# Kernel tuning notes

Measured on AMD Instinct MI355X. Metric: run time of the kernel, lower is better.

Reference implementation:

```python
import jax, jax.numpy as jnp
import numpy as np

NUM_HEADS = 16

def setup_inputs() -> dict:
    key = jax.random.key(0)
    ks = jax.random.split(key, 8)
    B, S, X, D = 2, 2048, 1, 1024
    scale = 1.0 / np.sqrt(D)
    return {
        "query": jax.random.normal(ks[0], (B, S, X, D), jnp.float32),
        "key": jax.random.normal(ks[1], (B, S, X, D), jnp.float32),
        "value": jax.random.normal(ks[2], (B, S, X, D), jnp.float32),
        "Wq": jax.random.normal(ks[3], (D, D), jnp.float32) * scale,
        "bq": jnp.zeros((D,), jnp.float32),
        "Wk": jax.random.normal(ks[4], (D, D), jnp.float32) * scale,
        "bk": jnp.zeros((D,), jnp.float32),
        "Wv": jax.random.normal(ks[5], (D, D), jnp.float32) * scale,
        "bv": jnp.zeros((D,), jnp.float32),
        "Wo": jax.random.normal(ks[6], (D, D), jnp.float32) * scale,
        "bo": jnp.zeros((D,), jnp.float32),
    }

def _split_heads(x, B, H):
    # [B, S, X, D] -> [B, H, S*X, depth]
    D = x.shape[-1]
    return x.reshape(B, -1, H, D // H).transpose(0, 2, 1, 3)

def reference(query, key, value, Wq, bq, Wk, bk, Wv, bv, Wo, bo):
    B, S, X, D = query.shape
    H = NUM_HEADS
    q = _split_heads(query @ Wq + bq, B, H)   # [B,H,L,dh], L=S*X
    k = _split_heads(key @ Wk + bk, B, H)
    v = _split_heads(value @ Wv + bv, B, H)
    dh = k.shape[-1]
    logits = jnp.einsum("bhqd,bhkd->bhqk", q, k) / jnp.sqrt(jnp.float32(dh))
    attn = jax.nn.softmax(logits, axis=-1)
    out = jnp.einsum("bhqk,bhkd->bhqd", attn, v)   # [B,H,L,dh]
    out = out.transpose(0, 2, 1, 3).reshape(B, S, -1, D)  # [B,S,X,D]
    return out @ Wo + bo
```

## Files before the change

### kernel.cpp

```cpp
#include <hip/hip_runtime.h>
#include <cstdint>
#include <cstddef>

typedef _Float16 f16x8 __attribute__((ext_vector_type(8)));
typedef __fp16 fp16x2 __attribute__((ext_vector_type(2)));
typedef float f32x4 __attribute__((ext_vector_type(4)));
typedef float f32x16 __attribute__((ext_vector_type(16)));
typedef unsigned short u16;
typedef unsigned int u32;

static constexpr int Bn = 2;
static constexpr int L  = 2048;
static constexpr int Dm = 1024;
static constexpr int H  = 16;
static constexpr int DH = 64;
static constexpr int M  = Bn * L;
static constexpr size_t PER = (size_t)Bn * H * L * DH;
static constexpr int NQ = Bn * H * L;

#define SC 0.18033688f

__device__ __forceinline__ u16 f2h(float f) {
    _Float16 h = (_Float16)f;
    u16 r; __builtin_memcpy(&r, &h, 2); return r;
}
__device__ __forceinline__ u32 pk_f16(float a, float b) {
    return (u32)f2h(a) | ((u32)f2h(b) << 16);
}
__device__ __forceinline__ u32 pk_rtz(float a, float b) {
#if __has_builtin(__builtin_amdgcn_cvt_pkrtz)
    fp16x2 t = __builtin_amdgcn_cvt_pkrtz(a, b);
    u32 r; __builtin_memcpy(&r, &t, 4); return r;
#else
    return pk_f16(a, b);
#endif
}

__device__ __forceinline__ void gl2lds16(const void* g, void* l) {
    __builtin_amdgcn_global_load_lds(
        (const __attribute__((address_space(1))) u32*)(uintptr_t)g,
        (__attribute__((address_space(3))) u32*)(uintptr_t)l, 16, 0, 0);
}

__device__ __forceinline__ void drain_vm() {
    asm volatile("s_waitcnt vmcnt(0)" ::: "memory");
}

__global__ __launch_bounds__(256) void convert_in(
    const float* __restrict__ q, const float* __restrict__ k, const float* __restrict__ v,
    u16* __restrict__ dst)
{
    const float* src = (blockIdx.y == 0) ? q : (blockIdx.y == 1) ? k : v;
    u16* d = dst + (size_t)blockIdx.y * M * Dm;
    const size_t t = (size_t)blockIdx.x * 256 + threadIdx.x;
    const float4* s4 = reinterpret_cast<const float4*>(src) + t * 2;
    float4 f0 = s4[0], f1 = s4[1];
    u32 o[4] = { pk_f16(f0.x, f0.y), pk_f16(f0.z, f0.w),
                 pk_f16(f1.x, f1.y), pk_f16(f1.z, f1.w) };
    reinterpret_cast<uint4*>(d)[t] = *reinterpret_cast<uint4*>(o);
}

__global__ __launch_bounds__(256) void convert_wt(
    const float* __restrict__ Wq, const float* __restrict__ Wk,
    const float* __restrict__ Wv, const float* __restrict__ Wo,
    u16* __restrict__ dst)
{
    __shared__ u16 Ts[64][72];
    const int z = blockIdx.z;
    const float* W = (z == 0) ? Wq : (z == 1) ? Wk : (z == 2) ? Wv : Wo;
    u16* o = dst + (size_t)z * Dm * Dm;
    const int n0 = blockIdx.x * 64, k0 = blockIdx.y * 64;
    const int tid = threadIdx.x;

    {
        const int kr = tid >> 2, nc = (tid & 3) * 16;
        const float* s = W + (size_t)(k0 + kr) * Dm + n0 + nc;
        const float4* s4 = reinterpret_cast<const float4*>(s);
        float4 a = s4[0], b = s4[1], c = s4[2], d = s4[3];
        u32 t[8] = { pk_f16(a.x, a.y), pk_f16(a.z, a.w), pk_f16(b.x, b.y), pk_f16(b.z, b.w),
                     pk_f16(c.x, c.y), pk_f16(c.z, c.w), pk_f16(d.x, d.y), pk_f16(d.z, d.w) };
        *reinterpret_cast<uint4*>(&Ts[kr][nc])     = reinterpret_cast<uint4*>(t)[0];
        *reinterpret_cast<uint4*>(&Ts[kr][nc + 8]) = reinterpret_cast<uint4*>(t)[1];
    }
    __syncthreads();
    {
        const int nr = tid >> 2, kc = (tid & 3) * 16;
        u16 w[16];
        #pragma unroll
        for (int j = 0; j < 16; ++j) w[j] = Ts[kc + j][nr];
        u16* dptr = o + (size_t)(n0 + nr) * Dm + k0 + kc;
        *reinterpret_cast<uint4*>(dptr)     = reinterpret_cast<uint4*>(w)[0];
        *reinterpret_cast<uint4*>(dptr + 8) = reinterpret_cast<uint4*>(w)[1];
    }
}

__global__ __launch_bounds__(256) void gemm_qkv(
    const u16* __restrict__ Abuf, const u16* __restrict__ Wtb,
    const float* __restrict__ bq, const float* __restrict__ bk, const float* __restrict__ bv,
    u16* __restrict__ Qh, u16* __restrict__ Kh, u16* __restrict__ Vth)
{
    __shared__ __align__(16) char smem[36864];

    const int tid = threadIdx.x;
    const int wave = tid >> 6, lane = tid & 63;
    const int quad = lane >> 4, l16 = lane & 15;
    const int wr = wave >> 1, wc = wave & 1;
    const int z = blockIdx.z;
    const u16* A  = Abuf + (size_t)z * M * Dm;
    const u16* Bt = Wtb  + (size_t)z * Dm * Dm;
    const float* bias = (z == 0) ? bq : (z == 1) ? bk : bv;
    u16* out = (z == 0) ? Qh : (z == 1) ? Kh : Vth;

    const int bid = blockIdx.y * 8 + blockIdx.x;
    const int m_idx = 4 * (bid & 7) + ((bid >> 3) & 3);
    const int n_idx = bid >> 5;
    const int n0 = n_idx * 128, m0 = m_idx * 128;

    const int srow = lane >> 2;
    const int skc  = (lane & 3) * 8;

    f32x4 acc[4][4] = {};

    auto stage = [&](int k0, int bi) {
        #pragma unroll
        for (int i = 0; i < 2; ++i) {
            const int ra = i * 64 + wave * 16;
            gl2lds16(A  + (size_t)(m0 + ra + srow) * Dm + k0 + skc, smem + bi * 8192 + ra * 64);
            gl2lds16(Bt + (size_t)(n0 + ra + srow) * Dm + k0 + skc, smem + 16384 + bi * 8192 + ra * 64);
        }
    };

    stage(0, 0);
    for (int k0 = 0, it = 0; k0 < Dm; k0 += 32, ++it) {
        const int cb = it & 1;
        __syncthreads();
        if (k0 + 32 < Dm) stage(k0 + 32, cb ^ 1);
        const u16* Asb = (const u16*)(smem + cb * 8192);
        const u16* Bsb = (const u16*)(smem + 16384 + cb * 8192);
        f16x8 af[4], bf[4];
        #pragma unroll
        for (int t = 0; t < 4; ++t) {
            af[t] = *reinterpret_cast<const f16x8*>(&Asb[(wr * 64 + t * 16 + l16) * 32 + quad * 8]);
            bf[t] = *reinterpret_cast<const f16x8*>(&Bsb[(wc * 64 + t * 16 + l16) * 32 + quad * 8]);
        }
        #pragma unroll
        for (int mt = 0; mt < 4; ++mt)
            #pragma unroll
            for (int nt = 0; nt < 4; ++nt)
                acc[mt][nt] = __builtin_amdgcn_mfma_f32_16x16x32_f16(af[mt], bf[nt], acc[mt][nt], 0, 0, 0);
    }

    __syncthreads();
    u16* tile = (u16*)smem + wave * 4608;
    const float qscale = (z == 0) ? SC : 1.0f;
    #pragma unroll
    for (int nt = 0; nt < 4; ++nt) {
        const int n = n0 + wc * 64 + nt * 16 + l16;
        const float badd = bias[n];
        const int cc = nt * 16 + l16;
        #pragma unroll
        for (int mt = 0; mt < 4; ++mt) {
            #pragma unroll
            for (int r = 0; r < 4; ++r) {
                const int rr = mt * 16 + quad * 4 + r;
                const u16 vv = f2h((acc[mt][nt][r] + badd) * qscale);
                if (z == 2) tile[cc * 72 + rr] = vv;
                else        tile[rr * 72 + cc] = vv;
            }
        }
    }
    __syncthreads();

    const int rsub = lane >> 3;
    const int csub = (lane & 7) * 8;
    const int h2 = (n0 + wc * 64) >> 6;
    const int mb = m0 + wr * 64;
    const int bb = mb >> 11, ll0 = mb & 2047;
    if (z == 2) {
        const size_t baseV = ((size_t)(bb * H + h2)) * DH * L;
        #pragma unroll
        for (int j = 0; j < 8; ++j) {
            const int d = j * 8 + rsub;
            uint4 vv = *reinterpret_cast<const uint4*>(&tile[d * 72 + csub]);
            *reinterpret_cast<uint4*>(out + baseV + (size_t)d * L + ll0 + csub) = vv;
        }
    } else {
        const size_t base = ((size_t)(bb * H + h2)) * L * DH;
        #pragma unroll
        for (int j = 0; j < 8; ++j) {
            const int row = j * 8 + rsub;
            uint4 vv = *reinterpret_cast<const uint4*>(&tile[row * 72 + csub]);
            *reinterpret_cast<uint4*>(out + base + (size_t)(ll0 + row) * DH + csub) = vv;
        }
    }
}

__global__ __launch_bounds__(256) void attn(
    const u16* __restrict__ Qh, const u16* __restrict__ Kh,
    const u16* __restrict__ Vth, u16* __restrict__ Opart, float* __restrict__ rsums)
{
    __shared__ __align__(16) char smem[32768];
    u16* Os = (u16*)smem;

    const int tid  = threadIdx.x;
    const int wave = tid >> 6, lane = tid & 63;
    const int l31  = lane & 31, hh = lane >> 5;

    const int bx  = blockIdx.x;
    const int hb  = (bx & 7) | ((bx >> 8) << 3);
    const int qth = (bx >> 3) & 31;
    const int h = hb & (H - 1), b = hb >> 4;
    const int qt = qth >> 1, half = qth & 1;

    const size_t hbase = ((size_t)(b * H + h)) * L * DH;
    const int q0 = qt * 128 + wave * 32;

    u16*  Op = Opart + (size_t)half * PER;
    float* rp = rsums + (size_t)half * NQ;

    f16x8 qf[4];
    {
        const u16* qp = Qh + hbase + (size_t)(q0 + l31) * DH + hh * 8;
        #pragma unroll
        for (int c = 0; c < 4; ++c)
            qf[c] = *reinterpret_cast<const f16x8*>(qp + c * 16);
    }

    f16x8 ones;
    {
        u32 ov[4] = { 0x3C003C00u, 0x3C003C00u, 0x3C003C00u, 0x3C003C00u };
        ones = *reinterpret_cast<f16x8*>(ov);
    }

    const int r_off = lane >> 3;
    const int s_sl  = lane & 7;

    auto stage = [&](int kt, int bi) {
        char* base = smem + bi * 16384;
        #pragma unroll
        for (int i = 0; i < 2; ++i) {
            const int rr = wave * 16 + i * 8 + r_off;
            gl2lds16(Kh  + hbase + (size_t)(kt * 64 + rr) * DH + ((s_sl ^ (rr & 7)) << 3),
                     base + (wave * 16 + i * 8) * 128);
            gl2lds16(Vth + hbase + (size_t)rr * L + kt * 64 + ((s_sl ^ (rr & 7)) << 3),
                     base + 8192 + (wave * 16 + i * 8) * 128);
        }
    };

    int vbK[2], vbV[2];
    #pragma unroll
    for (int t = 0; t < 2; ++t) {
        const int rr = t * 32 + l31;
        vbK[t] = rr * 128 + ((rr & 7) << 4);
        vbV[t] = 8192 + rr * 128 + ((rr & 7) << 4);
    }

    f32x16 oacc[2] = {};
    f32x16 oaccR = {};

    const int kt0 = half * 16;
    stage(kt0, 0);
    for (int ktl = 0; ktl < 16; ++ktl) {
        const int cb = ktl & 1;
        drain_vm();
        __syncthreads();
        if (ktl + 1 < 16) stage(kt0 + ktl + 1, cb ^ 1);
        const char* ldsb = smem + cb * 16384;

        f32x16 st[2] = {};
        #pragma unroll
        for (int t = 0; t < 2; ++t) {
            #pragma unroll
            for (int c = 0; c < 4; ++c) {
                f16x8 kf = *reinterpret_cast<const f16x8*>(ldsb + (vbK[t] ^ (((c << 1) | hh) << 4)));
                st[t] = __builtin_amdgcn_mfma_f32_32x32x16_f16(kf, qf[c], st[t], 0, 0, 0);
            }
        }

        f16x8 pfrag[4];
        #pragma unroll
        for (int t = 0; t < 2; ++t) {
            float p[16];
            #pragma unroll
            for (int rr = 0; rr < 16; ++rr)
                p[rr] = __builtin_amdgcn_exp2f(st[t][rr]);
            #pragma unroll
            for (int g = 0; g < 2; ++g) {
                float* pg = p + g * 8;
                u32 w0 = pk_rtz(pg[0], pg[1]);
                u32 w1 = pk_rtz(pg[2], pg[3]);
                u32 w2 = pk_rtz(pg[4], pg[5]);
                u32 w3 = pk_rtz(pg[6], pg[7]);
                asm volatile("v_permlane32_swap_b32 %0, %1" : "+v"(w0), "+v"(w2));
                asm volatile("v_permlane32_swap_b32 %0, %1" : "+v"(w1), "+v"(w3));
                u32 pkv[4] = { w0, w1, w2, w3 };
                pfrag[t * 2 + g] = *reinterpret_cast<f16x8*>(pkv);
            }
        }

        #pragma unroll
        for (int c = 0; c < 4; ++c) {
            #pragma unroll
            for (int t = 0; t < 2; ++t) {
                f16x8 vf = *reinterpret_cast<const f16x8*>(ldsb + (vbV[t] ^ (((c << 1) | hh) << 4)));
                oacc[t] = __builtin_amdgcn_mfma_f32_32x32x16_f16(vf, pfrag[c], oacc[t], 0, 0, 0);
            }
            oaccR = __builtin_amdgcn_mfma_f32_32x32x16_f16(ones, pfrag[c], oaccR, 0, 0, 0);
        }
    }

    drain_vm();
    #pragma unroll
    for (int pass = 0; pass < 2; ++pass) {
        __syncthreads();
        if ((wave >> 1) == pass) {
            const int qloc = (wave & 1) * 32 + l31;
            #pragma unroll
            for (int t = 0; t < 2; ++t) {
                #pragma unroll
                for (int rq = 0; rq < 4; ++rq) {
                    const int d0 = t * 32 + rq * 8 + hh * 4;
                    *reinterpret_cast<u32*>(&Os[qloc * 72 + d0]) =
                        pk_f16(oacc[t][rq * 4 + 0], oacc[t][rq * 4 + 1]);
                    *reinterpret_cast<u32*>(&Os[qloc * 72 + d0 + 2]) =
                        pk_f16(oacc[t][rq * 4 + 2], oacc[t][rq * 4 + 3]);
                }
            }
        }
        __syncthreads();
        {
            const int row = tid >> 2, cc = (tid & 3) * 16;
            u16* dst = Op + hbase + (size_t)(qt * 128 + pass * 64 + row) * DH + cc;
            *reinterpret_cast<uint4*>(dst)     = *reinterpret_cast<const uint4*>(&Os[row * 72 + cc]);
            *reinterpret_cast<uint4*>(dst + 8) = *reinterpret_cast<const uint4*>(&Os[row * 72 + cc + 8]);
        }
    }
    if (hh == 0) rp[((size_t)(b * H + h)) * L + q0 + l31] = oaccR[0];
}

__global__ __launch_bounds__(256) void attn_merge(
    const u16* __restrict__ O0, const u16* __restrict__ O1,
    const float* __restrict__ r0, const float* __restrict__ r1,
    u16* __restrict__ ctx)
{
    const int g = blockIdx.x * 256 + threadIdx.x;
    const int row = g >> 3, dc = (g & 7) * 8;
    const int b = row >> 15, h = (row >> 11) & (H - 1), l = row & (L - 1);
    const float inv = 1.0f / (r0[row] + r1[row]);
    f16x8 a = *reinterpret_cast<const f16x8*>(O0 + (size_t)row * DH + dc);
    f16x8 c = *reinterpret_cast<const f16x8*>(O1 + (size_t)row * DH + dc);
    u32 o[4];
    #pragma unroll
    for (int i = 0; i < 4; ++i)
        o[i] = pk_f16(((float)a[2 * i] + (float)c[2 * i]) * inv,
                      ((float)a[2 * i + 1] + (float)c[2 * i + 1]) * inv);
    *reinterpret_cast<uint4*>(ctx + ((size_t)(b * L + l)) * Dm + h * DH + dc) =
        *reinterpret_cast<uint4*>(o);
}

__global__ __launch_bounds__(512) void gemm_out(
    const u16* __restrict__ A, const u16* __restrict__ Bt,
    const float* __restrict__ bias, float* __restrict__ out)
{
    __shared__ u16 As[2][128 * 32];
    __shared__ u16 Bs[2][128 * 32];
    const int tid = threadIdx.x;
    const int wave = tid >> 6, lane = tid & 63;
    const int quad = lane >> 4, l16 = lane & 15;
    const int wr = wave >> 1, wc = wave & 1;
    const int n0 = blockIdx.x * 128, m0 = blockIdx.y * 128;

    const int srow = lane >> 2;
    const int skc  = (lane & 3) * 8;

    f32x4 acc[2][4] = {};

    auto stage = [&](int k0, int bi) {
        gl2lds16(A  + (size_t)(m0 + wave * 16 + srow) * Dm + k0 + skc, &As[bi][(wave * 16) * 32]);
        gl2lds16(Bt + (size_t)(n0 + wave * 16 + srow) * Dm + k0 + skc, &Bs[bi][(wave * 16) * 32]);
    };

    stage(0, 0);
    for (int k0 = 0, it = 0; k0 < Dm; k0 += 32, ++it) {
        const int cb = it & 1;
        __syncthreads();
        if (k0 + 32 < Dm) stage(k0 + 32, cb ^ 1);
        f16x8 af[2], bf[4];
        #pragma unroll
        for (int t = 0; t < 2; ++t)
            af[t] = *reinterpret_cast<const f16x8*>(&As[cb][(wr * 32 + t * 16 + l16) * 32 + quad * 8]);
        #pragma unroll
        for (int t = 0; t < 4; ++t)
            bf[t] = *reinterpret_cast<const f16x8*>(&Bs[cb][(wc * 64 + t * 16 + l16) * 32 + quad * 8]);
        #pragma unroll
        for (int mt = 0; mt < 2; ++mt)
            #pragma unroll
            for (int nt = 0; nt < 4; ++nt)
                acc[mt][nt] = __builtin_amdgcn_mfma_f32_16x16x32_f16(af[mt], bf[nt], acc[mt][nt], 0, 0, 0);
    }

    #pragma unroll
    for (int nt = 0; nt < 4; ++nt) {
        const int n = n0 + wc * 64 + nt * 16 + l16;
        const float badd = bias[n];
        #pragma unroll
        for (int mt = 0; mt < 2; ++mt) {
            #pragma unroll
            for (int r = 0; r < 4; ++r) {
                const int m = m0 + wr * 32 + mt * 16 + quad * 4 + r;
                out[(size_t)m * Dm + n] = acc[mt][nt][r] + badd;
            }
        }
    }
}

extern "C" void kernel_launch(void* const* d_in, const int* in_sizes, int n_in,
                              void* d_out, int out_size, void* d_ws, size_t ws_size,
                              hipStream_t stream) {
    const float* q  = (const float*)d_in[0];
    const float* k  = (const float*)d_in[1];
    const float* v  = (const float*)d_in[2];
    const float* Wq = (const float*)d_in[3];
    const float* bq = (const float*)d_in[4];
    const float* Wk = (const float*)d_in[5];
    const float* bk = (const float*)d_in[6];
    const float* Wv = (const float*)d_in[7];
    const float* bv = (const float*)d_in[8];
    const float* Wo = (const float*)d_in[9];
    const float* bo = (const float*)d_in[10];
    float* out = (float*)d_out;

    u16* Abuf = (u16*)d_ws;
    u16* Wt   = Abuf + 3 * (size_t)M * Dm;
    u16* Qh   = Wt + 4 * (size_t)Dm * Dm;
    u16* Kh   = Qh + PER;
    u16* Vth  = Kh + PER;
    u16* O0   = Vth + PER;
    float* rs = (float*)(O0 + 2 * PER);
    u16* ctx  = Abuf;

    convert_in <<<dim3((M * Dm) / 8 / 256, 3), 256, 0, stream>>>(q, k, v, Abuf);
    convert_wt <<<dim3(Dm / 64, Dm / 64, 4), 256, 0, stream>>>(Wq, Wk, Wv, Wo, Wt);
    gemm_qkv   <<<dim3(Dm / 128, M / 128, 3), 256, 0, stream>>>(Abuf, Wt, bq, bk, bv, Qh, Kh, Vth);
    attn       <<<dim3(L / 128 * 2 * H * Bn), 256, 0, stream>>>(Qh, Kh, Vth, O0, rs);
    attn_merge <<<NQ * 8 / 256, 256, 0, stream>>>(O0, O0 + PER, rs, rs + NQ, ctx);
    gemm_out   <<<dim3(Dm / 128, M / 128), 512, 0, stream>>>(ctx, Wt + 3 * (size_t)Dm * Dm, bo, out);
}
```

Before: 231.4 us.

## Fuse input fp16 conversion into QKV GEMM and attention merge into output GEMM

Removes the separate convert_in and attn_merge kernels. The QKV GEMM now loads fp32 activations through registers and converts them to fp16 before writing to LDS, and the output GEMM reads the two partial attention outputs plus row sums, normalizes them and writes the A tile itself. This saves two launches and the round trips through the intermediate buffers. In exchange, A-tile loads lose the async global-to-LDS path and need a full vmcnt drain each iteration, and A data is re-read and re-converted by every N-tile block, so global traffic for A rises.

```diff
diff --git a/kernel.cpp b/kernel.cpp
--- a/kernel.cpp
+++ b/kernel.cpp
@@ -44,20 +44,6 @@
 
 __device__ __forceinline__ void drain_vm() {
     asm volatile("s_waitcnt vmcnt(0)" ::: "memory");
-}
-
-__global__ __launch_bounds__(256) void convert_in(
-    const float* __restrict__ q, const float* __restrict__ k, const float* __restrict__ v,
-    u16* __restrict__ dst)
-{
-    const float* src = (blockIdx.y == 0) ? q : (blockIdx.y == 1) ? k : v;
-    u16* d = dst + (size_t)blockIdx.y * M * Dm;
-    const size_t t = (size_t)blockIdx.x * 256 + threadIdx.x;
-    const float4* s4 = reinterpret_cast<const float4*>(src) + t * 2;
-    float4 f0 = s4[0], f1 = s4[1];
-    u32 o[4] = { pk_f16(f0.x, f0.y), pk_f16(f0.z, f0.w),
-                 pk_f16(f1.x, f1.y), pk_f16(f1.z, f1.w) };
-    reinterpret_cast<uint4*>(d)[t] = *reinterpret_cast<uint4*>(o);
 }
 
 __global__ __launch_bounds__(256) void convert_wt(
@@ -95,7 +81,8 @@
 }
 
 __global__ __launch_bounds__(256) void gemm_qkv(
-    const u16* __restrict__ Abuf, const u16* __restrict__ Wtb,
+    const float* __restrict__ qx, const float* __restrict__ kx, const float* __restrict__ vx,
+    const u16* __restrict__ Wtb,
     const float* __restrict__ bq, const float* __restrict__ bk, const float* __restrict__ bv,
     u16* __restrict__ Qh, u16* __restrict__ Kh, u16* __restrict__ Vth)
 {
@@ -106,8 +93,8 @@
     const int quad = lane >> 4, l16 = lane & 15;
     const int wr = wave >> 1, wc = wave & 1;
     const int z = blockIdx.z;
-    const u16* A  = Abuf + (size_t)z * M * Dm;
-    const u16* Bt = Wtb  + (size_t)z * Dm * Dm;
+    const float* Asrc = (z == 0) ? qx : (z == 1) ? kx : vx;
+    const u16* Bt = Wtb + (size_t)z * Dm * Dm;
     const float* bias = (z == 0) ? bq : (z == 1) ? bk : bv;
     u16* out = (z == 0) ? Qh : (z == 1) ? Kh : Vth;
 
@@ -121,20 +108,45 @@
 
     f32x4 acc[4][4] = {};
 
-    auto stage = [&](int k0, int bi) {
+    auto stageA_load = [&](int k0, float4* r) {
         #pragma unroll
         for (int i = 0; i < 2; ++i) {
             const int ra = i * 64 + wave * 16;
-            gl2lds16(A  + (size_t)(m0 + ra + srow) * Dm + k0 + skc, smem + bi * 8192 + ra * 64);
-            gl2lds16(Bt + (size_t)(n0 + ra + srow) * Dm + k0 + skc, smem + 16384 + bi * 8192 + ra * 64);
-        }
-    };
-
-    stage(0, 0);
+            const float* s = Asrc + (size_t)(m0 + ra + srow) * Dm + k0 + skc;
+            r[2 * i]     = *reinterpret_cast<const float4*>(s);
+            r[2 * i + 1] = *reinterpret_cast<const float4*>(s + 4);
+        }
+    };
+    auto stageA_write = [&](int bi, const float4* r) {
+        #pragma unroll
+        for (int i = 0; i < 2; ++i) {
+            const int ra = i * 64 + wave * 16;
+            u32 o[4] = { pk_f16(r[2 * i].x,     r[2 * i].y),
+                         pk_f16(r[2 * i].z,     r[2 * i].w),
+                         pk_f16(r[2 * i + 1].x, r[2 * i + 1].y),
+                         pk_f16(r[2 * i + 1].z, r[2 * i + 1].w) };
+            *reinterpret_cast<uint4*>(smem + bi * 8192 + (ra + srow) * 64 + skc * 2) =
+                *reinterpret_cast<uint4*>(o);
+        }
+    };
+    auto stageB = [&](int k0, int bi) {
+        #pragma unroll
+        for (int i = 0; i < 2; ++i) {
+            const int ra = i * 64 + wave * 16;
+            gl2lds16(Bt + (size_t)(n0 + ra + srow) * Dm + k0 + skc,
+                     smem + 16384 + bi * 8192 + ra * 64);
+        }
+    };
+
+    float4 areg[4];
+    stageA_load(0, areg);
+    stageB(0, 0);
+    stageA_write(0, areg);
     for (int k0 = 0, it = 0; k0 < Dm; k0 += 32, ++it) {
         const int cb = it & 1;
+        drain_vm();
         __syncthreads();
-        if (k0 + 32 < Dm) stage(k0 + 32, cb ^ 1);
+        if (k0 + 32 < Dm) { stageA_load(k0 + 32, areg); stageB(k0 + 32, cb ^ 1); }
         const u16* Asb = (const u16*)(smem + cb * 8192);
         const u16* Bsb = (const u16*)(smem + 16384 + cb * 8192);
         f16x8 af[4], bf[4];
@@ -148,6 +160,7 @@
             #pragma unroll
             for (int nt = 0; nt < 4; ++nt)
                 acc[mt][nt] = __builtin_amdgcn_mfma_f32_16x16x32_f16(af[mt], bf[nt], acc[mt][nt], 0, 0, 0);
+        if (k0 + 32 < Dm) stageA_write(cb ^ 1, areg);
     }
 
     __syncthreads();
@@ -338,29 +351,10 @@
     if (hh == 0) rp[((size_t)(b * H + h)) * L + q0 + l31] = oaccR[0];
 }
 
-__global__ __launch_bounds__(256) void attn_merge(
+__global__ __launch_bounds__(512) void gemm_out(
     const u16* __restrict__ O0, const u16* __restrict__ O1,
     const float* __restrict__ r0, const float* __restrict__ r1,
-    u16* __restrict__ ctx)
-{
-    const int g = blockIdx.x * 256 + threadIdx.x;
-    const int row = g >> 3, dc = (g & 7) * 8;
-    const int b = row >> 15, h = (row >> 11) & (H - 1), l = row & (L - 1);
-    const float inv = 1.0f / (r0[row] + r1[row]);
-    f16x8 a = *reinterpret_cast<const f16x8*>(O0 + (size_t)row * DH + dc);
-    f16x8 c = *reinterpret_cast<const f16x8*>(O1 + (size_t)row * DH + dc);
-    u32 o[4];
-    #pragma unroll
-    for (int i = 0; i < 4; ++i)
-        o[i] = pk_f16(((float)a[2 * i] + (float)c[2 * i]) * inv,
-                      ((float)a[2 * i + 1] + (float)c[2 * i + 1]) * inv);
-    *reinterpret_cast<uint4*>(ctx + ((size_t)(b * L + l)) * Dm + h * DH + dc) =
-        *reinterpret_cast<uint4*>(o);
-}
-
-__global__ __launch_bounds__(512) void gemm_out(
-    const u16* __restrict__ A, const u16* __restrict__ Bt,
-    const float* __restrict__ bias, float* __restrict__ out)
+    const u16* __restrict__ Bt, const float* __restrict__ bias, float* __restrict__ out)
 {
     __shared__ u16 As[2][128 * 32];
     __shared__ u16 Bs[2][128 * 32];
@@ -375,16 +369,43 @@
 
     f32x4 acc[2][4] = {};
 
-    auto stage = [&](int k0, int bi) {
-        gl2lds16(A  + (size_t)(m0 + wave * 16 + srow) * Dm + k0 + skc, &As[bi][(wave * 16) * 32]);
+    const int m  = m0 + wave * 16 + srow;
+    const int bb = m >> 11, ll = m & 2047;
+
+    auto stageA_load = [&](int k0, uint4& a0, uint4& a1, float& inv) {
+        const int k = k0 + skc;
+        const int h = k >> 6, d = k & 63;
+        const size_t ridx  = ((size_t)(bb * H + h)) * L + ll;
+        const size_t obase = ridx * DH + d;
+        a0 = *reinterpret_cast<const uint4*>(O0 + obase);
+        a1 = *reinterpret_cast<const uint4*>(O1 + obase);
+        inv = 1.0f / (r0[ridx] + r1[ridx]);
+    };
+    auto stageA_write = [&](int bi, uint4 a0, uint4 a1, float inv) {
+        f16x8 x0, x1;
+        __builtin_memcpy(&x0, &a0, 16);
+        __builtin_memcpy(&x1, &a1, 16);
+        u32 o[4];
+        #pragma unroll
+        for (int i = 0; i < 4; ++i)
+            o[i] = pk_f16(((float)x0[2 * i] + (float)x1[2 * i]) * inv,
+                          ((float)x0[2 * i + 1] + (float)x1[2 * i + 1]) * inv);
+        *reinterpret_cast<uint4*>(&As[bi][(wave * 16 + srow) * 32 + skc]) =
+            *reinterpret_cast<uint4*>(o);
+    };
+    auto stageB = [&](int k0, int bi) {
         gl2lds16(Bt + (size_t)(n0 + wave * 16 + srow) * Dm + k0 + skc, &Bs[bi][(wave * 16) * 32]);
     };
 
-    stage(0, 0);
+    uint4 a0r, a1r; float ainv;
+    stageA_load(0, a0r, a1r, ainv);
+    stageB(0, 0);
+    stageA_write(0, a0r, a1r, ainv);
     for (int k0 = 0, it = 0; k0 < Dm; k0 += 32, ++it) {
         const int cb = it & 1;
+        drain_vm();
         __syncthreads();
-        if (k0 + 32 < Dm) stage(k0 + 32, cb ^ 1);
+        if (k0 + 32 < Dm) { stageA_load(k0 + 32, a0r, a1r, ainv); stageB(k0 + 32, cb ^ 1); }
         f16x8 af[2], bf[4];
         #pragma unroll
         for (int t = 0; t < 2; ++t)
@@ -397,6 +418,7 @@
             #pragma unroll
             for (int nt = 0; nt < 4; ++nt)
                 acc[mt][nt] = __builtin_amdgcn_mfma_f32_16x16x32_f16(af[mt], bf[nt], acc[mt][nt], 0, 0, 0);
+        if (k0 + 32 < Dm) stageA_write(cb ^ 1, a0r, a1r, ainv);
     }
 
     #pragma unroll
@@ -407,8 +429,8 @@
         for (int mt = 0; mt < 2; ++mt) {
             #pragma unroll
             for (int r = 0; r < 4; ++r) {
-                const int m = m0 + wr * 32 + mt * 16 + quad * 4 + r;
-                out[(size_t)m * Dm + n] = acc[mt][nt][r] + badd;
+                const int mm = m0 + wr * 32 + mt * 16 + quad * 4 + r;
+                out[(size_t)mm * Dm + n] = acc[mt][nt][r] + badd;
             }
         }
     }
@@ -430,19 +452,16 @@
     const float* bo = (const float*)d_in[10];
     float* out = (float*)d_out;
 
-    u16* Abuf = (u16*)d_ws;
-    u16* Wt   = Abuf + 3 * (size_t)M * Dm;
+    u16* Wt   = (u16*)d_ws;
     u16* Qh   = Wt + 4 * (size_t)Dm * Dm;
     u16* Kh   = Qh + PER;
     u16* Vth  = Kh + PER;
     u16* O0   = Vth + PER;
     float* rs = (float*)(O0 + 2 * PER);
-    u16* ctx  = Abuf;
-
-    convert_in <<<dim3((M * Dm) / 8 / 256, 3), 256, 0, stream>>>(q, k, v, Abuf);
+
     convert_wt <<<dim3(Dm / 64, Dm / 64, 4), 256, 0, stream>>>(Wq, Wk, Wv, Wo, Wt);
-    gemm_qkv   <<<dim3(Dm / 128, M / 128, 3), 256, 0, stream>>>(Abuf, Wt, bq, bk, bv, Qh, Kh, Vth);
+    gemm_qkv   <<<dim3(Dm / 128, M / 128, 3), 256, 0, stream>>>(q, k, v, Wt, bq, bk, bv, Qh, Kh, Vth);
     attn       <<<dim3(L / 128 * 2 * H * Bn), 256, 0, stream>>>(Qh, Kh, Vth, O0, rs);
-    attn_merge <<<NQ * 8 / 256, 256, 0, stream>>>(O0, O0 + PER, rs, rs + NQ, ctx);
-    gemm_out   <<<dim3(Dm / 128, M / 128), 512, 0, stream>>>(ctx, Wt + 3 * (size_t)Dm * Dm, bo, out);
-}
+    gemm_out   <<<dim3(Dm / 128, M / 128), 512, 0, stream>>>(O0, O0 + PER, rs, rs + NQ,
+                                                             Wt + 3 * (size_t)Dm * Dm, bo, out);
+}
```

New measurement: 242.9 us. 5.0% more time.

## Fuse split-attention merge into output projection GEMM A-tile staging

Applied to the files above, without the earlier changes.

Removes the separate attn_merge kernel and performs the merge (sum of two partial outputs scaled by the inverse row-sum) while staging the A tile in gemm_out, reading O0/O1 and row sums directly through registers and writing them to LDS after the MFMA block. This drops one kernel launch and the ctx round trip through global memory. In exchange each gemm_out block redoes the merge for its A rows once per N-tile (8x redundant reads of O0/O1) and uses register-staged loads. It also adds explicit vm drains before barriers in gemm_qkv and the loop, which may serialize async LDS loads.

```diff
diff --git a/kernel.cpp b/kernel.cpp
--- a/kernel.cpp
+++ b/kernel.cpp
@@ -133,6 +133,7 @@
     stage(0, 0);
     for (int k0 = 0, it = 0; k0 < Dm; k0 += 32, ++it) {
         const int cb = it & 1;
+        drain_vm();
         __syncthreads();
         if (k0 + 32 < Dm) stage(k0 + 32, cb ^ 1);
         const u16* Asb = (const u16*)(smem + cb * 8192);
@@ -150,6 +151,7 @@
                 acc[mt][nt] = __builtin_amdgcn_mfma_f32_16x16x32_f16(af[mt], bf[nt], acc[mt][nt], 0, 0, 0);
     }
 
+    drain_vm();
     __syncthreads();
     u16* tile = (u16*)smem + wave * 4608;
     const float qscale = (z == 0) ? SC : 1.0f;
@@ -338,29 +340,10 @@
     if (hh == 0) rp[((size_t)(b * H + h)) * L + q0 + l31] = oaccR[0];
 }
 
-__global__ __launch_bounds__(256) void attn_merge(
+__global__ __launch_bounds__(512) void gemm_out(
     const u16* __restrict__ O0, const u16* __restrict__ O1,
     const float* __restrict__ r0, const float* __restrict__ r1,
-    u16* __restrict__ ctx)
-{
-    const int g = blockIdx.x * 256 + threadIdx.x;
-    const int row = g >> 3, dc = (g & 7) * 8;
-    const int b = row >> 15, h = (row >> 11) & (H - 1), l = row & (L - 1);
-    const float inv = 1.0f / (r0[row] + r1[row]);
-    f16x8 a = *reinterpret_cast<const f16x8*>(O0 + (size_t)row * DH + dc);
-    f16x8 c = *reinterpret_cast<const f16x8*>(O1 + (size_t)row * DH + dc);
-    u32 o[4];
-    #pragma unroll
-    for (int i = 0; i < 4; ++i)
-        o[i] = pk_f16(((float)a[2 * i] + (float)c[2 * i]) * inv,
-                      ((float)a[2 * i + 1] + (float)c[2 * i + 1]) * inv);
-    *reinterpret_cast<uint4*>(ctx + ((size_t)(b * L + l)) * Dm + h * DH + dc) =
-        *reinterpret_cast<uint4*>(o);
-}
-
-__global__ __launch_bounds__(512) void gemm_out(
-    const u16* __restrict__ A, const u16* __restrict__ Bt,
-    const float* __restrict__ bias, float* __restrict__ out)
+    const u16* __restrict__ Bt, const float* __restrict__ bias, float* __restrict__ out)
 {
     __shared__ u16 As[2][128 * 32];
     __shared__ u16 Bs[2][128 * 32];
@@ -375,16 +358,43 @@
 
     f32x4 acc[2][4] = {};
 
-    auto stage = [&](int k0, int bi) {
-        gl2lds16(A  + (size_t)(m0 + wave * 16 + srow) * Dm + k0 + skc, &As[bi][(wave * 16) * 32]);
+    const int m  = m0 + wave * 16 + srow;
+    const int bb = m >> 11, ll = m & 2047;
+
+    auto stageA_load = [&](int k0, uint4& a0, uint4& a1, float& inv) {
+        const int k = k0 + skc;
+        const int h = k >> 6, d = k & 63;
+        const size_t ridx  = ((size_t)(bb * H + h)) * L + ll;
+        const size_t obase = ridx * DH + d;
+        a0 = *reinterpret_cast<const uint4*>(O0 + obase);
+        a1 = *reinterpret_cast<const uint4*>(O1 + obase);
+        inv = 1.0f / (r0[ridx] + r1[ridx]);
+    };
+    auto stageA_write = [&](int bi, uint4 a0, uint4 a1, float inv) {
+        f16x8 x0, x1;
+        __builtin_memcpy(&x0, &a0, 16);
+        __builtin_memcpy(&x1, &a1, 16);
+        u32 o[4];
+        #pragma unroll
+        for (int i = 0; i < 4; ++i)
+            o[i] = pk_f16(((float)x0[2 * i] + (float)x1[2 * i]) * inv,
+                          ((float)x0[2 * i + 1] + (float)x1[2 * i + 1]) * inv);
+        *reinterpret_cast<uint4*>(&As[bi][(wave * 16 + srow) * 32 + skc]) =
+            *reinterpret_cast<uint4*>(o);
+    };
+    auto stageB = [&](int k0, int bi) {
         gl2lds16(Bt + (size_t)(n0 + wave * 16 + srow) * Dm + k0 + skc, &Bs[bi][(wave * 16) * 32]);
     };
 
-    stage(0, 0);
+    uint4 a0r, a1r; float ainv;
+    stageA_load(0, a0r, a1r, ainv);
+    stageB(0, 0);
+    stageA_write(0, a0r, a1r, ainv);
     for (int k0 = 0, it = 0; k0 < Dm; k0 += 32, ++it) {
         const int cb = it & 1;
+        drain_vm();
         __syncthreads();
-        if (k0 + 32 < Dm) stage(k0 + 32, cb ^ 1);
+        if (k0 + 32 < Dm) { stageA_load(k0 + 32, a0r, a1r, ainv); stageB(k0 + 32, cb ^ 1); }
         f16x8 af[2], bf[4];
         #pragma unroll
         for (int t = 0; t < 2; ++t)
@@ -397,6 +407,7 @@
             #pragma unroll
             for (int nt = 0; nt < 4; ++nt)
                 acc[mt][nt] = __builtin_amdgcn_mfma_f32_16x16x32_f16(af[mt], bf[nt], acc[mt][nt], 0, 0, 0);
+        if (k0 + 32 < Dm) stageA_write(cb ^ 1, a0r, a1r, ainv);
     }
 
     #pragma unroll
@@ -407,8 +418,8 @@
         for (int mt = 0; mt < 2; ++mt) {
             #pragma unroll
             for (int r = 0; r < 4; ++r) {
-                const int m = m0 + wr * 32 + mt * 16 + quad * 4 + r;
-                out[(size_t)m * Dm + n] = acc[mt][nt][r] + badd;
+                const int mm = m0 + wr * 32 + mt * 16 + quad * 4 + r;
+                out[(size_t)mm * Dm + n] = acc[mt][nt][r] + badd;
             }
         }
     }
@@ -437,12 +448,11 @@
     u16* Vth  = Kh + PER;
     u16* O0   = Vth + PER;
     float* rs = (float*)(O0 + 2 * PER);
-    u16* ctx  = Abuf;
 
     convert_in <<<dim3((M * Dm) / 8 / 256, 3), 256, 0, stream>>>(q, k, v, Abuf);
     convert_wt <<<dim3(Dm / 64, Dm / 64, 4), 256, 0, stream>>>(Wq, Wk, Wv, Wo, Wt);
     gemm_qkv   <<<dim3(Dm / 128, M / 128, 3), 256, 0, stream>>>(Abuf, Wt, bq, bk, bv, Qh, Kh, Vth);
     attn       <<<dim3(L / 128 * 2 * H * Bn), 256, 0, stream>>>(Qh, Kh, Vth, O0, rs);
-    attn_merge <<<NQ * 8 / 256, 256, 0, stream>>>(O0, O0 + PER, rs, rs + NQ, ctx);
-    gemm_out   <<<dim3(Dm / 128, M / 128), 512, 0, stream>>>(ctx, Wt + 3 * (size_t)Dm * Dm, bo, out);
-}
+    gemm_out   <<<dim3(Dm / 128, M / 128), 512, 0, stream>>>(O0, O0 + PER, rs, rs + NQ,
+                                                             Wt + 3 * (size_t)Dm * Dm, bo, out);
+}
```

After: 237.9 us. 2.8% more time.
